# Kernel tuning notes

Hardware: AMD Instinct MI355X
Metric: run time of the kernel (lower is better)

The kernel has to match this reference:

```python
import jax, jax.numpy as jnp
import numpy as np

MARGIN = 0.3
EPS = 1e-8  # torch CosineSimilarity eps

N, D = 16384, 256


def setup_inputs() -> dict:
    key = jax.random.key(0)
    k1, k2 = jax.random.split(key)
    x = jax.random.normal(k1, (N, D), dtype=jnp.float32)
    y = jax.random.normal(k2, (N, D), dtype=jnp.float32)
    return {"x": x, "y": y}


def _cosine_matrix(x, y):
    # torch cosine_similarity: dot / max(|x||y|, eps). Normalize rows with eps clamp.
    xn = x / jnp.maximum(jnp.linalg.norm(x, axis=-1, keepdims=True), EPS)
    yn = y / jnp.maximum(jnp.linalg.norm(y, axis=-1, keepdims=True), EPS)
    return xn @ yn.T  # [N, N]


def _rank(S):
    # S[i, j] = cos(x_i, y_j). Positive pair on diagonal.
    diag = jnp.diagonal(S)                      # [N]
    E = jnp.exp(S)                              # [N, N]
    neg_sum = jnp.sum(E, axis=1) - jnp.exp(diag)  # sum over n != i of exp(cos(x_i, y_n))
    m = jnp.exp(diag - MARGIN)                  # margin only on positive term
    ret = m / (m + neg_sum)
    return -jnp.mean(ret)


def reference(x, y):
    S = _cosine_matrix(x, y)
    # bidirectional: rank(x, y) + rank(y, x); rank(y, x) uses transposed sims
    return _rank(S) + _rank(S.T)
```

## Files before the change

### kernel.cpp

```cpp
#include <hip/hip_runtime.h>

#define N_ROWS 16384
#define DIM 256
#define MARGINF 0.3f
#define CH 2048
#define NT 64
#define LOG2E 1.44269504089f

typedef float f32x4 __attribute__((ext_vector_type(4)));
typedef int i32x4 __attribute__((ext_vector_type(4)));
typedef int i32x8 __attribute__((ext_vector_type(8)));
typedef long lng;

__device__ __forceinline__ float fexp2(float x) {
#if __has_builtin(__builtin_amdgcn_exp2f)
  return __builtin_amdgcn_exp2f(x);
#else
  return exp2f(x);
#endif
}

__device__ __forceinline__ unsigned char to_e4m3(float f) {
  unsigned u = __float_as_uint(f);
  unsigned sign = (u >> 24) & 0x80u;
  float a = fabsf(f);
  if (a >= 448.0f) return (unsigned char)(sign | 0x7eu);
  if (a < 0.015625f) {
    int q = (int)(a * 512.0f + 0.5f);
    return (unsigned char)(sign | (unsigned)q);
  }
  int e;
  float m = frexpf(a, &e);
  float mant = 2.0f * m;
  int e8 = e - 1;
  int mb = (int)(mant * 8.0f + 0.5f) - 8;
  if (mb == 8) { mb = 0; ++e8; if (e8 > 8) return (unsigned char)(sign | 0x7eu); }
  return (unsigned char)(sign | (unsigned)((e8 + 7) << 3) | (unsigned)mb);
}

__device__ __forceinline__ unsigned int pack4_e4m3(float a, float b, float c, float d) {
#if __has_builtin(__builtin_amdgcn_cvt_pk_fp8_f32)
  int lo = __builtin_amdgcn_cvt_pk_fp8_f32(a, b, 0, false);
  int r = __builtin_amdgcn_cvt_pk_fp8_f32(c, d, lo, true);
  return (unsigned int)r;
#else
  return (unsigned int)to_e4m3(a) | ((unsigned int)to_e4m3(b) << 8) |
         ((unsigned int)to_e4m3(c) << 16) | ((unsigned int)to_e4m3(d) << 24);
#endif
}

__global__ __launch_bounds__(256) void normalize_kernel(
    const float* __restrict__ x, const float* __restrict__ y,
    unsigned int* __restrict__ xn8, unsigned int* __restrict__ yn8,
    float* __restrict__ diagF) {
  const int wid = threadIdx.x >> 6;
  const int lane = threadIdx.x & 63;
  const int r = blockIdx.x * 4 + wid;
  const float4 vx = *reinterpret_cast<const float4*>(x + (size_t)r * DIM + lane * 4);
  const float4 vy = *reinterpret_cast<const float4*>(y + (size_t)r * DIM + lane * 4);
  float sx = vx.x * vx.x + vx.y * vx.y + vx.z * vx.z + vx.w * vx.w;
  float sy = vy.x * vy.x + vy.y * vy.y + vy.z * vy.z + vy.w * vy.w;
  float sxy = vx.x * vy.x + vx.y * vy.y + vx.z * vy.z + vx.w * vy.w;
  #pragma unroll
  for (int off = 32; off; off >>= 1) {
    sx += __shfl_xor(sx, off);
    sy += __shfl_xor(sy, off);
    sxy += __shfl_xor(sxy, off);
  }
  const float scx = LOG2E / fmaxf(sqrtf(sx), 1e-8f);
  const float scy = 1.0f / fmaxf(sqrtf(sy), 1e-8f);
  if (lane == 0) diagF[r] = sxy * (scx / LOG2E) * scy;
  xn8[(size_t)r * 64 + lane] = pack4_e4m3(vx.x * scx, vx.y * scx, vx.z * scx, vx.w * scx);
  yn8[(size_t)r * 64 + lane] = pack4_e4m3(vy.x * scy, vy.y * scy, vy.z * scy, vy.w * scy);
}

__device__ __forceinline__ void stage_wave(const unsigned char* __restrict__ src,
                                           int colBase32, unsigned char* slab, int lane) {
  #pragma unroll
  for (int it = 0; it < 8; ++it) {
    const int id = it * 64 + lane;
    const int col = id >> 4;
    const int slot = id & 15;
    const unsigned char* gp =
        src + (unsigned)((colBase32 + col) * DIM + ((slot ^ (col & 7)) << 4));
    unsigned char* l = slab + it * 1024;
    __builtin_amdgcn_global_load_lds(
        (const __attribute__((address_space(1))) unsigned int*)gp,
        (__attribute__((address_space(3))) unsigned int*)l, 16, 0, 0);
  }
}

__global__ __launch_bounds__(256, 2) void gemm_exp_kernel(
    const unsigned char* __restrict__ xn8, const unsigned char* __restrict__ yn8,
    float* __restrict__ rowpart, float* __restrict__ colpartW,
    float* __restrict__ rowsumG, float* __restrict__ colsumG, int use_scratch) {
  __shared__ unsigned char lds[4][2][8192];

  const int tid = threadIdx.x;
  const int lane = tid & 63;
  const int wid = tid >> 6;
  const int grp = lane >> 4, li = lane & 15;

  const int bid = blockIdx.x;
  const int chunk = bid & 7;
  const int band = (bid >> 3) * 4 + wid;
  const int rowBase = band * 64;
  const int colBase = chunk * CH;

  i32x8 a[4][2];
  #pragma unroll
  for (int m = 0; m < 4; ++m)
    #pragma unroll
    for (int kb = 0; kb < 2; ++kb) {
      const int row = rowBase + m * 16 + li;
      a[m][kb] = *reinterpret_cast<const i32x8*>(
          xn8 + (size_t)row * DIM + kb * 128 + grp * 32);
    }

  float rsum[4][4];
  #pragma unroll
  for (int m = 0; m < 4; ++m)
    #pragma unroll
    for (int j = 0; j < 4; ++j) rsum[m][j] = 0.0f;

  unsigned char* slab0 = &lds[wid][0][0];
  unsigned char* slab1 = &lds[wid][1][0];
  const int sw = li & 7;
  const int g2 = grp * 2;

  stage_wave(yn8, colBase, slab0, lane);
  __builtin_amdgcn_sched_barrier(0);

  for (int t = 0; t < NT; ++t) {
    if (t + 1 < NT)
      stage_wave(yn8, colBase + (t + 1) * 32, (t & 1) ? slab0 : slab1, lane);
    __builtin_amdgcn_sched_barrier(0);
    if (t == 0)          asm volatile("s_waitcnt vmcnt(8)" ::: "memory");
    else if (t + 1 < NT) asm volatile("s_waitcnt vmcnt(10)" ::: "memory");
    else                 asm volatile("s_waitcnt vmcnt(2)" ::: "memory");
    __builtin_amdgcn_sched_barrier(0);

    const unsigned char* Bp = (t & 1) ? slab1 : slab0;
    const unsigned char* colp0 = Bp + (size_t)li * 256;
    const unsigned char* colp1 = Bp + (size_t)(li + 16) * 256;
    f32x4 acc[4][2];
    #pragma unroll
    for (int m = 0; m < 4; ++m) { acc[m][0] = (f32x4)(0.0f); acc[m][1] = (f32x4)(0.0f); }

    __builtin_amdgcn_s_setprio(1);
    #pragma unroll
    for (int kb = 0; kb < 2; ++kb) {
      const int s0 = ((kb * 8 + g2) ^ sw) << 4;
      const int s1 = ((kb * 8 + g2 + 1) ^ sw) << 4;
      const i32x4 b0lo = *reinterpret_cast<const i32x4*>(colp0 + s0);
      const i32x4 b0hi = *reinterpret_cast<const i32x4*>(colp0 + s1);
      const i32x4 b1lo = *reinterpret_cast<const i32x4*>(colp1 + s0);
      const i32x4 b1hi = *reinterpret_cast<const i32x4*>(colp1 + s1);
      const i32x8 b0 = __builtin_shufflevector(b0lo, b0hi, 0, 1, 2, 3, 4, 5, 6, 7);
      const i32x8 b1 = __builtin_shufflevector(b1lo, b1hi, 0, 1, 2, 3, 4, 5, 6, 7);
      #pragma unroll
      for (int m = 0; m < 4; ++m) {
        acc[m][0] = __builtin_amdgcn_mfma_scale_f32_16x16x128_f8f6f4(
            a[m][kb], b0, acc[m][0], 0, 0, 0, 127, 0, 127);
        acc[m][1] = __builtin_amdgcn_mfma_scale_f32_16x16x128_f8f6f4(
            a[m][kb], b1, acc[m][1], 0, 0, 0, 127, 0, 127);
      }
    }
    __builtin_amdgcn_s_setprio(0);

    float cs0 = 0.0f, cs1 = 0.0f;
    #pragma unroll
    for (int m = 0; m < 4; ++m) {
      #pragma unroll
      for (int j = 0; j < 4; ++j) {
        const float e0 = fexp2(acc[m][0][j]);
        const float e1 = fexp2(acc[m][1][j]);
        rsum[m][j] += e0 + e1;
        cs0 += e0;
        cs1 += e1;
      }
    }
    cs0 += __shfl_xor(cs0, 16); cs0 += __shfl_xor(cs0, 32);
    cs1 += __shfl_xor(cs1, 16); cs1 += __shfl_xor(cs1, 32);
    if (grp == 0) {
      const int c = colBase + t * 32 + li;
      if (use_scratch) {
        colpartW[(size_t)band * N_ROWS + c] = cs0;
        colpartW[(size_t)band * N_ROWS + c + 16] = cs1;
      } else {
        atomicAdd(&colsumG[c], cs0);
        atomicAdd(&colsumG[c + 16], cs1);
      }
    }
  }

  #pragma unroll
  for (int m = 0; m < 4; ++m) {
    #pragma unroll
    for (int j = 0; j < 4; ++j) {
      float v = rsum[m][j];
      v += __shfl_xor(v, 1); v += __shfl_xor(v, 2);
      v += __shfl_xor(v, 4); v += __shfl_xor(v, 8);
      if (li == 0) {
        const int r = rowBase + m * 16 + grp * 4 + j;
        if (use_scratch) rowpart[(size_t)chunk * N_ROWS + r] = v;
        else atomicAdd(&rowsumG[r], v);
      }
    }
  }
}

__global__ __launch_bounds__(256) void finalize_kernel(
    const float* __restrict__ rowpart, const float* __restrict__ colpartW,
    const float* __restrict__ rowsumG, const float* __restrict__ colsumG,
    const float* __restrict__ diagF, float* __restrict__ out, int use_scratch) {
  __shared__ float red[4];
  const int i = blockIdx.x * 256 + threadIdx.x;
  float rs, cs;
  if (use_scratch) {
    rs = 0.0f;
    #pragma unroll
    for (int c = 0; c < 8; ++c) rs += rowpart[(size_t)c * N_ROWS + i];
    cs = 0.0f;
    #pragma unroll 8
    for (int b = 0; b < 256; ++b) cs += colpartW[(size_t)b * N_ROWS + i];
  } else {
    rs = rowsumG[i];
    cs = colsumG[i];
  }
  const float d = diagF[i];
  const float e8 = fexp2(LOG2E * d);
  const float mm = __expf(d - MARGINF);
  float v = mm / (mm + rs - e8) + mm / (mm + cs - e8);
  #pragma unroll
  for (int off = 32; off; off >>= 1) v += __shfl_xor(v, off);
  if ((threadIdx.x & 63) == 0) red[threadIdx.x >> 6] = v;
  __syncthreads();
  if (threadIdx.x == 0) {
    const float t = red[0] + red[1] + red[2] + red[3];
    atomicAdd(out, -t / (float)N_ROWS);
  }
}

extern "C" void kernel_launch(void* const* d_in, const int* in_sizes, int n_in,
                              void* d_out, int out_size, void* d_ws, size_t ws_size,
                              hipStream_t stream) {
  const float* x = (const float*)d_in[0];
  const float* y = (const float*)d_in[1];
  char* ws = (char*)d_ws;
  unsigned char* xn8 = (unsigned char*)ws;
  unsigned char* yn8 = (unsigned char*)(ws + (4u << 20));
  float* diagF    = (float*)(ws + (8u << 20));
  float* rowpart  = (float*)(ws + (8u << 20) + 65536);
  float* colpartW = (float*)(ws + (8u << 20) + 65536 + 524288);
  float* rowsumG = rowpart;
  float* colsumG = rowpart + N_ROWS;
  const size_t need_scratch = (8u << 20) + 65536 + 524288 + (16u << 20);
  const int use_scratch = (ws_size >= need_scratch) ? 1 : 0;

  hipMemsetAsync(d_out, 0, sizeof(float), stream);
  if (!use_scratch) hipMemsetAsync(rowsumG, 0, 2 * N_ROWS * sizeof(float), stream);
  normalize_kernel<<<4096, 256, 0, stream>>>(x, y, (unsigned int*)xn8,
                                             (unsigned int*)yn8, diagF);
  gemm_exp_kernel<<<512, 256, 0, stream>>>(xn8, yn8, rowpart, colpartW,
                                           rowsumG, colsumG, use_scratch);
  finalize_kernel<<<64, 256, 0, stream>>>(rowpart, colpartW, rowsumG, colsumG,
                                          diagF, (float*)d_out, use_scratch);
}
```

Measured before the change: 126.8 us.

## Halve per-wave column tile and double grid with XCD-aware chunk mapping

Shrinks the per-iteration column tile from 32 to 16 columns and the column chunk from 2048 to 1024, which doubles the grid to 1024 blocks and halves the LDS slab per wave. Block-to-chunk mapping now groups two chunks per XCD, so blocks on one XCD share the same y columns in their L2. The aim is more blocks and occupancy, fewer registers, and better L2 locality. The cost is half the MFMA work per B load and twice as many partial row sums to reduce in finalize.

```diff
diff --git a/kernel.cpp b/kernel.cpp
--- a/kernel.cpp
+++ b/kernel.cpp
@@ -3,14 +3,13 @@
 #define N_ROWS 16384
 #define DIM 256
 #define MARGINF 0.3f
-#define CH 2048
+#define CH 1024
 #define NT 64
 #define LOG2E 1.44269504089f
 
 typedef float f32x4 __attribute__((ext_vector_type(4)));
 typedef int i32x4 __attribute__((ext_vector_type(4)));
 typedef int i32x8 __attribute__((ext_vector_type(8)));
-typedef long lng;
 
 __device__ __forceinline__ float fexp2(float x) {
 #if __has_builtin(__builtin_amdgcn_exp2f)
@@ -75,14 +74,14 @@
 }
 
 __device__ __forceinline__ void stage_wave(const unsigned char* __restrict__ src,
-                                           int colBase32, unsigned char* slab, int lane) {
-  #pragma unroll
-  for (int it = 0; it < 8; ++it) {
+                                           int colBase16, unsigned char* slab, int lane) {
+  #pragma unroll
+  for (int it = 0; it < 4; ++it) {
     const int id = it * 64 + lane;
     const int col = id >> 4;
     const int slot = id & 15;
     const unsigned char* gp =
-        src + (unsigned)((colBase32 + col) * DIM + ((slot ^ (col & 7)) << 4));
+        src + (unsigned)((colBase16 + col) * DIM + ((slot ^ (col & 7)) << 4));
     unsigned char* l = slab + it * 1024;
     __builtin_amdgcn_global_load_lds(
         (const __attribute__((address_space(1))) unsigned int*)gp,
@@ -94,7 +93,7 @@
     const unsigned char* __restrict__ xn8, const unsigned char* __restrict__ yn8,
     float* __restrict__ rowpart, float* __restrict__ colpartW,
     float* __restrict__ rowsumG, float* __restrict__ colsumG, int use_scratch) {
-  __shared__ unsigned char lds[4][2][8192];
+  __shared__ unsigned char lds[4][2][4096];
 
   const int tid = threadIdx.x;
   const int lane = tid & 63;
@@ -102,8 +101,10 @@
   const int grp = lane >> 4, li = lane & 15;
 
   const int bid = blockIdx.x;
-  const int chunk = bid & 7;
-  const int band = (bid >> 3) * 4 + wid;
+  const int xcd = bid & 7;
+  const int rest = bid >> 3;
+  const int chunk = xcd * 2 + (rest >> 6);
+  const int band = ((rest & 63) << 2) + wid;
   const int rowBase = band * 64;
   const int colBase = chunk * CH;
 
@@ -133,64 +134,50 @@
 
   for (int t = 0; t < NT; ++t) {
     if (t + 1 < NT)
-      stage_wave(yn8, colBase + (t + 1) * 32, (t & 1) ? slab0 : slab1, lane);
+      stage_wave(yn8, colBase + (t + 1) * 16, (t & 1) ? slab0 : slab1, lane);
     __builtin_amdgcn_sched_barrier(0);
-    if (t == 0)          asm volatile("s_waitcnt vmcnt(8)" ::: "memory");
-    else if (t + 1 < NT) asm volatile("s_waitcnt vmcnt(10)" ::: "memory");
-    else                 asm volatile("s_waitcnt vmcnt(2)" ::: "memory");
+    if (t == 0)          asm volatile("s_waitcnt vmcnt(4)" ::: "memory");
+    else if (t + 1 < NT) asm volatile("s_waitcnt vmcnt(5)" ::: "memory");
+    else                 asm volatile("s_waitcnt vmcnt(1)" ::: "memory");
     __builtin_amdgcn_sched_barrier(0);
 
     const unsigned char* Bp = (t & 1) ? slab1 : slab0;
-    const unsigned char* colp0 = Bp + (size_t)li * 256;
-    const unsigned char* colp1 = Bp + (size_t)(li + 16) * 256;
-    f32x4 acc[4][2];
-    #pragma unroll
-    for (int m = 0; m < 4; ++m) { acc[m][0] = (f32x4)(0.0f); acc[m][1] = (f32x4)(0.0f); }
+    const unsigned char* colp = Bp + (size_t)li * 256;
+    f32x4 acc[4];
+    #pragma unroll
+    for (int m = 0; m < 4; ++m) acc[m] = (f32x4)(0.0f);
 
     __builtin_amdgcn_s_setprio(1);
     #pragma unroll
     for (int kb = 0; kb < 2; ++kb) {
       const int s0 = ((kb * 8 + g2) ^ sw) << 4;
       const int s1 = ((kb * 8 + g2 + 1) ^ sw) << 4;
-      const i32x4 b0lo = *reinterpret_cast<const i32x4*>(colp0 + s0);
-      const i32x4 b0hi = *reinterpret_cast<const i32x4*>(colp0 + s1);
-      const i32x4 b1lo = *reinterpret_cast<const i32x4*>(colp1 + s0);
-      const i32x4 b1hi = *reinterpret_cast<const i32x4*>(colp1 + s1);
-      const i32x8 b0 = __builtin_shufflevector(b0lo, b0hi, 0, 1, 2, 3, 4, 5, 6, 7);
-      const i32x8 b1 = __builtin_shufflevector(b1lo, b1hi, 0, 1, 2, 3, 4, 5, 6, 7);
+      const i32x4 blo = *reinterpret_cast<const i32x4*>(colp + s0);
+      const i32x4 bhi = *reinterpret_cast<const i32x4*>(colp + s1);
+      const i32x8 b = __builtin_shufflevector(blo, bhi, 0, 1, 2, 3, 4, 5, 6, 7);
       #pragma unroll
-      for (int m = 0; m < 4; ++m) {
-        acc[m][0] = __builtin_amdgcn_mfma_scale_f32_16x16x128_f8f6f4(
-            a[m][kb], b0, acc[m][0], 0, 0, 0, 127, 0, 127);
-        acc[m][1] = __builtin_amdgcn_mfma_scale_f32_16x16x128_f8f6f4(
-            a[m][kb], b1, acc[m][1], 0, 0, 0, 127, 0, 127);
-      }
+      for (int m = 0; m < 4; ++m)
+        acc[m] = __builtin_amdgcn_mfma_scale_f32_16x16x128_f8f6f4(
+            a[m][kb], b, acc[m], 0, 0, 0, 127, 0, 127);
     }
     __builtin_amdgcn_s_setprio(0);
 
-    float cs0 = 0.0f, cs1 = 0.0f;
+    float cs = 0.0f;
     #pragma unroll
     for (int m = 0; m < 4; ++m) {
       #pragma unroll
       for (int j = 0; j < 4; ++j) {
-        const float e0 = fexp2(acc[m][0][j]);
-        const float e1 = fexp2(acc[m][1][j]);
-        rsum[m][j] += e0 + e1;
-        cs0 += e0;
-        cs1 += e1;
+        const float e = fexp2(acc[m][j]);
+        rsum[m][j] += e;
+        cs += e;
       }
     }
-    cs0 += __shfl_xor(cs0, 16); cs0 += __shfl_xor(cs0, 32);
-    cs1 += __shfl_xor(cs1, 16); cs1 += __shfl_xor(cs1, 32);
+    cs += __shfl_xor(cs, 16);
+    cs += __shfl_xor(cs, 32);
     if (grp == 0) {
-      const int c = colBase + t * 32 + li;
-      if (use_scratch) {
-        colpartW[(size_t)band * N_ROWS + c] = cs0;
-        colpartW[(size_t)band * N_ROWS + c + 16] = cs1;
-      } else {
-        atomicAdd(&colsumG[c], cs0);
-        atomicAdd(&colsumG[c + 16], cs1);
-      }
+      const int c = colBase + t * 16 + li;
+      if (use_scratch) colpartW[(size_t)band * N_ROWS + c] = cs;
+      else atomicAdd(&colsumG[c], cs);
     }
   }
 
@@ -220,7 +207,7 @@
   if (use_scratch) {
     rs = 0.0f;
     #pragma unroll
-    for (int c = 0; c < 8; ++c) rs += rowpart[(size_t)c * N_ROWS + i];
+    for (int c = 0; c < 16; ++c) rs += rowpart[(size_t)c * N_ROWS + i];
     cs = 0.0f;
     #pragma unroll 8
     for (int b = 0; b < 256; ++b) cs += colpartW[(size_t)b * N_ROWS + i];
@@ -252,18 +239,18 @@
   unsigned char* yn8 = (unsigned char*)(ws + (4u << 20));
   float* diagF    = (float*)(ws + (8u << 20));
   float* rowpart  = (float*)(ws + (8u << 20) + 65536);
-  float* colpartW = (float*)(ws + (8u << 20) + 65536 + 524288);
+  float* colpartW = (float*)(ws + (8u << 20) + 65536 + (1u << 20));
   float* rowsumG = rowpart;
   float* colsumG = rowpart + N_ROWS;
-  const size_t need_scratch = (8u << 20) + 65536 + 524288 + (16u << 20);
+  const size_t need_scratch = (8u << 20) + 65536 + (1u << 20) + (16u << 20);
   const int use_scratch = (ws_size >= need_scratch) ? 1 : 0;
 
   hipMemsetAsync(d_out, 0, sizeof(float), stream);
   if (!use_scratch) hipMemsetAsync(rowsumG, 0, 2 * N_ROWS * sizeof(float), stream);
   normalize_kernel<<<4096, 256, 0, stream>>>(x, y, (unsigned int*)xn8,
                                              (unsigned int*)yn8, diagF);
-  gemm_exp_kernel<<<512, 256, 0, stream>>>(xn8, yn8, rowpart, colpartW,
-                                           rowsumG, colsumG, use_scratch);
+  gemm_exp_kernel<<<1024, 256, 0, stream>>>(xn8, yn8, rowpart, colpartW,
+                                            rowsumG, colsumG, use_scratch);
   finalize_kernel<<<64, 256, 0, stream>>>(rowpart, colpartW, rowsumG, colsumG,
                                           diagF, (float*)d_out, use_scratch);
 }
```

Measured after the change: 118.9 us. 6.3% less time.
